# Kernel optimization log

Measured on AMD Instinct MI355X. Metric: run time of the kernel, lower is better.

## Reference

```python
import jax, jax.numpy as jnp
import numpy as np

NUM_HEADS = 16
KEY_DIM = 64
D_MODEL = 1024
SUPPORTS = 128


def _gaussian_orthogonal_random_matrix(m, d, seed=0):
    # GOR sampler with scaling=0: orthogonal blocks, rows rescaled by norms of iid Gaussian rows.
    rng = np.random.RandomState(seed)
    blocks = []
    n_full = m // d
    for _ in range(n_full):
        q, _ = np.linalg.qr(rng.randn(d, d))
        blocks.append(q.T)
    rem = m - n_full * d
    if rem > 0:
        q, _ = np.linalg.qr(rng.randn(d, d))
        blocks.append(q.T[:rem])
    W = np.concatenate(blocks, axis=0)  # [m, d], orthonormal rows per block
    multiplier = np.linalg.norm(rng.randn(m, d), axis=1)  # chi(d) row norms
    return (multiplier[:, None] * W).astype(np.float32)


def setup_inputs() -> dict:
    key0 = jax.random.key(0)
    ks = jax.random.split(key0, 12)
    B, S, D, H, K = 4, 4096, D_MODEL, NUM_HEADS, KEY_DIM
    glorot_in = lambda k, shape, fan_in, fan_out: jax.random.uniform(
        k, shape, jnp.float32, -1.0, 1.0) * np.sqrt(6.0 / (fan_in + fan_out))
    return {
        "query": jax.random.normal(ks[0], (B, S, D), jnp.float32),
        "value": jax.random.normal(ks[1], (B, S, D), jnp.float32),
        "key": jax.random.normal(ks[2], (B, S, D), jnp.float32),
        "Wq": glorot_in(ks[3], (D, H, K), D, H * K),
        "bq": jnp.zeros((H, K), jnp.float32),
        "Wk": glorot_in(ks[4], (D, H, K), D, H * K),
        "bk": jnp.zeros((H, K), jnp.float32),
        "Wv": glorot_in(ks[5], (D, H, K), D, H * K),
        "bv": jnp.zeros((H, K), jnp.float32),
        "Wo": glorot_in(ks[6], (H, K, D), H * K, D),
        "bo": jnp.zeros((D,), jnp.float32),
        "proj": jnp.asarray(_gaussian_orthogonal_random_matrix(SUPPORTS, K)),
    }


def kernel_feature_creator(data, projection, is_query):
    # FAVOR+ positive softmax-kernel features: phi(x) = exp(w.x' - |x'|^2/2 - stab)/sqrt(m)
    d = data.shape[-1]
    m = projection.shape[0]
    x = data * (d ** -0.25)  # so that q'.k' = q.k / sqrt(d)
    wx = jnp.einsum("bshk,mk->bshm", x, projection)
    diag = 0.5 * jnp.sum(x * x, axis=-1, keepdims=True)
    if is_query:
        stab = jax.lax.stop_gradient(jnp.max(wx, axis=-1, keepdims=True))
    else:
        stab = jax.lax.stop_gradient(jnp.max(wx))
    return jnp.exp(wx - diag - stab) * (m ** -0.5)


def reference(query, value, key, Wq, bq, Wk, bk, Wv, bv, Wo, bo, proj):
    # EinsumDense projections: [B,S,D] -> [B,S,H,K]
    q = jnp.einsum("bsd,dhk->bshk", query, Wq) + bq
    k = jnp.einsum("bsd,dhk->bshk", key, Wk) + bk
    v = jnp.einsum("bsd,dhk->bshk", value, Wv) + bv
    phi_q = kernel_feature_creator(q, proj, True)   # [B,T,H,M]
    phi_k = kernel_feature_creator(k, proj, False)  # [B,S,H,M]
    kv = jnp.einsum("bshm,bshd->bhmd", phi_k, v)
    qkv = jnp.einsum("bthm,bhmd->bthd", phi_q, kv)
    # normalisation: D = phi_q . (sum_s phi_k)
    k1 = jnp.sum(phi_k, axis=1)                     # [B,H,M]
    denom = jnp.einsum("bthm,bhm->bth", phi_q, k1)
    out = qkv * (1.0 / (denom + 1e-6))[..., None]
    return jnp.einsum("bthd,hdo->bto", out, Wo) + bo
```

## Files before the change

### kernel.cpp

```cpp
#include <hip/hip_runtime.h>
#include <hip/hip_bf16.h>


#define B_  4
#define S_  4096
#define H_  16

#define SCALE_X 0.3535533905932738f
#define CM      0.08838834764831845f

typedef __attribute__((ext_vector_type(8))) short bf16x8;
typedef __attribute__((ext_vector_type(4))) short s16x4;
typedef __attribute__((ext_vector_type(8))) unsigned short u16x8;
typedef __attribute__((ext_vector_type(8))) _Float16 f16x8;
typedef __attribute__((ext_vector_type(4))) _Float16 f16x4;
typedef __attribute__((ext_vector_type(4))) float f32x4;

#define OFF_A    ((size_t)0)
#define OFF_B    ((size_t)16777216)
#define OFF_X    ((size_t)33554432)
#define OFF_KV   ((size_t)37814272)
#define OFF_K1   ((size_t)38338560)
#define OFF_BM   ((size_t)38346752)
#define OFF_ST   ((size_t)38347264)
#define OFF_A16  ((size_t)38347776)

__device__ __forceinline__ unsigned short f2bf(float x) {
  union { __hip_bfloat16 b; unsigned short u; } c;
  c.b = __float2bfloat16(x);
  return c.u;
}

#define MFMAB(ACC, A, B)                                               \
  ACC = __builtin_amdgcn_mfma_f32_16x16x32_bf16(A, B, ACC, 0, 0, 0)

#define GLDS(GP, LP)                                                  \
  __builtin_amdgcn_global_load_lds(                                   \
      (const __attribute__((address_space(1))) unsigned int*)(GP),    \
      (__attribute__((address_space(3))) unsigned int*)(LP), 16, 0, 0)

__device__ __forceinline__ void load_pfrag(const float* __restrict__ proj, int m,
                                           int kb, bf16x8* ph) {
  const float* p = proj + m * 64 + kb;
  float4 a = *reinterpret_cast<const float4*>(p);
  float4 b = *reinterpret_cast<const float4*>(p + 4);
  float v[8] = {a.x, a.y, a.z, a.w, b.x, b.y, b.z, b.w};
  bf16x8 h;
#pragma unroll
  for (int j = 0; j < 8; ++j) h[j] = (short)f2bf(v[j]);
  *ph = h;
}

#define STAGE_XR(XV, WANT_DIAG)                                           \
  {                                                                       \
    f16x8 xv_ = (XV);                                                     \
    u16x8 hh_;                                                            \
    float sq_ = 0.f;                                                      \
    _Pragma("unroll") for (int j = 0; j < 8; ++j) {                       \
      float vf_ = (float)xv_[j] * SCALE_X;                                \
      sq_ += vf_ * vf_;                                                   \
      hh_[j] = f2bf(vf_);                                                 \
    }                                                                     \
    *reinterpret_cast<u16x8*>(&Xh[srow][xc]) = hh_;                       \
    if (WANT_DIAG) {                                                      \
      sq_ += __shfl_xor(sq_, 1);                                          \
      sq_ += __shfl_xor(sq_, 2);                                          \
      sq_ += __shfl_xor(sq_, 4);                                          \
      if ((tid & 7) == 0) diags[srow] = 0.5f * sq_;                       \
    }                                                                     \
  }

#define WX_COMPUTE(WX)                                                       \
  _Pragma("unroll") for (int st_ = 0; st_ < 2; ++st_)                        \
  _Pragma("unroll") for (int ks_ = 0; ks_ < 2; ++ks_) {                      \
    const int rr_ = st_ * 16 + l15;                                          \
    const int cc_ = ((ks_ * 4 + lg) ^ (l15 & 7)) << 3;                       \
    bf16x8 xh_ = *reinterpret_cast<const bf16x8*>(&Xh[rr_][cc_]);            \
    _Pragma("unroll") for (int mtl_ = 0; mtl_ < 2; ++mtl_)                   \
        MFMAB(WX[st_][mtl_], xh_, ph[mtl_][ks_]);                            \
  }

__global__ __launch_bounds__(256) void cvt_f16_kernel(
    const float* __restrict__ in, _Float16* __restrict__ out) {
  const size_t stride = (size_t)gridDim.x * 256 * 8;
  for (size_t i = ((size_t)blockIdx.x * 256 + threadIdx.x) * 8; i < 16777216UL;
       i += stride) {
    float4 a = *reinterpret_cast<const float4*>(in + i);
    float4 b = *reinterpret_cast<const float4*>(in + i + 4);
    f16x8 h;
    h[0] = (_Float16)a.x; h[1] = (_Float16)a.y;
    h[2] = (_Float16)a.z; h[3] = (_Float16)a.w;
    h[4] = (_Float16)b.x; h[5] = (_Float16)b.y;
    h[6] = (_Float16)b.z; h[7] = (_Float16)b.w;
    *reinterpret_cast<f16x8*>(out + i) = h;
  }
}

__global__ __launch_bounds__(256) void wt_f16_kernel(
    const float* __restrict__ W, _Float16* __restrict__ T) {
  __shared__ float t[32][33];
  const int tx = threadIdx.x & 31, ty = threadIdx.x >> 5;
  const int k0 = blockIdx.x * 32, n0 = blockIdx.y * 32;
#pragma unroll
  for (int i = 0; i < 4; ++i)
    t[ty + 8 * i][tx] = W[(size_t)(k0 + ty + 8 * i) * 1024 + n0 + tx];
  __syncthreads();
#pragma unroll
  for (int i = 0; i < 4; ++i)
    T[(size_t)(n0 + ty + 8 * i) * 1024 + k0 + tx] = (_Float16)t[tx][ty + 8 * i];
}

template <int F16OUT>
__global__ __launch_bounds__(512) void gemm_lds(
    const _Float16* __restrict__ A16, const _Float16* __restrict__ BT,
    const float* __restrict__ bias, void* __restrict__ Cout) {
  __shared__ _Float16 As[4][256][32];
  __shared__ _Float16 Bs[4][256][32];
  const int tid = threadIdx.x;
  const int bid = blockIdx.x;
  const int m0 = (bid & 63) << 8;
  const int n0 = (bid >> 6) << 8;
  const int wave = tid >> 6, lane = tid & 63;
  const int wm = (wave >> 2) << 7;
  const int wn = (wave & 3) << 6;
  const int l15 = lane & 15, lg = lane >> 4;

  const int rlo = tid >> 2;
  const int cg = ((tid & 3) ^ ((rlo >> 1) & 3)) << 3;
  const int wqbase = wave << 10;

  const _Float16* pa = A16 + (size_t)(m0 + rlo) * 1024 + cg;
  const _Float16* pb = BT + (size_t)(n0 + rlo) * 1024 + cg;

  f32x4 acc[8][4];
#pragma unroll
  for (int i = 0; i < 8; ++i)
#pragma unroll
    for (int j = 0; j < 4; ++j) acc[i][j] = f32x4{0.f, 0.f, 0.f, 0.f};

#define STAGE_T(nb, kt)                                                   \
  {                                                                       \
    char* la = (char*)&As[nb][0][0] + wqbase;                             \
    char* lb = (char*)&Bs[nb][0][0] + wqbase;                             \
    GLDS(pa + (kt) * 32, la);                                             \
    GLDS(pa + (kt) * 32 + 131072, la + 8192);                             \
    GLDS(pb + (kt) * 32, lb);                                             \
    GLDS(pb + (kt) * 32 + 131072, lb + 8192);                             \
  }

#define PIPE_BAR(N)                                                       \
  asm volatile("s_waitcnt vmcnt(" #N ")" ::: "memory");                   \
  __builtin_amdgcn_s_barrier();                                           \
  asm volatile("" ::: "memory");                                          \
  __builtin_amdgcn_sched_barrier(0);

#define COMPUTE(cur)                                                      \
  {                                                                       \
    f16x8 bf[4];                                                          \
    _Pragma("unroll") for (int fn = 0; fn < 4; ++fn) {                    \
      const int r = wn + fn * 16 + l15;                                   \
      bf[fn] = *reinterpret_cast<const f16x8*>(                           \
          &Bs[cur][r][(lg ^ ((r >> 1) & 3)) << 3]);                       \
    }                                                                     \
    _Pragma("unroll") for (int fm = 0; fm < 8; ++fm) {                    \
      const int r = wm + fm * 16 + l15;                                   \
      f16x8 av = *reinterpret_cast<const f16x8*>(                         \
          &As[cur][r][(lg ^ ((r >> 1) & 3)) << 3]);                       \
      _Pragma("unroll") for (int fn = 0; fn < 4; ++fn)                    \
        acc[fm][fn] = __builtin_amdgcn_mfma_f32_16x16x32_f16(             \
            av, bf[fn], acc[fm][fn], 0, 0, 0);                            \
    }                                                                     \
  }

  STAGE_T(0, 0);
  STAGE_T(1, 1);

  for (int kt = 0; kt < 30; ++kt) {
    STAGE_T((kt + 2) & 3, kt + 2);
    PIPE_BAR(8);
    COMPUTE(kt & 3);
  }
  PIPE_BAR(4);
  COMPUTE(2);
  PIPE_BAR(0);
  COMPUTE(3);

#pragma unroll
  for (int fm = 0; fm < 8; ++fm) {
    const int row = m0 + wm + fm * 16 + (lg << 2);
#pragma unroll
    for (int fn = 0; fn < 4; ++fn) {
      const int col = n0 + wn + fn * 16 + l15;
      const float bc = bias[col];
      f32x4 v = acc[fm][fn];
      if (F16OUT) {
        _Float16* C = (_Float16*)Cout;
#pragma unroll
        for (int j = 0; j < 4; ++j)
          C[(size_t)(row + j) * 1024 + col] = (_Float16)(v[j] + bc);
      } else {
        float* C = (float*)Cout;
#pragma unroll
        for (int j = 0; j < 4; ++j) C[(size_t)(row + j) * 1024 + col] = v[j] + bc;
      }
    }
  }
#undef STAGE_T
#undef PIPE_BAR
#undef COMPUTE
}

__global__ __launch_bounds__(256) void wxmax_mfma_kernel(
    const _Float16* __restrict__ kproj, const float* __restrict__ proj,
    float* __restrict__ blockmax) {
  __shared__ unsigned short Xh[32][64];
  __shared__ float diags[32];
  __shared__ float redw[4];
  const int tid = threadIdx.x, blk = blockIdx.x;
  const int lane = tid & 63, w = tid >> 6;
  const int l15 = lane & 15, lg = lane >> 4;
  (void)diags;

  bf16x8 ph[2][2];
#pragma unroll
  for (int mtl = 0; mtl < 2; ++mtl)
#pragma unroll
    for (int ks = 0; ks < 2; ++ks)
      load_pfrag(proj, (2 * w + mtl) * 16 + l15, ks * 32 + lg * 8, &ph[mtl][ks]);

  float gmax = -3.4e38f;
  const int srow = tid >> 3, q8 = (tid & 7) << 3;
  const int xc = ((q8 >> 3) ^ (srow & 7)) << 3;

  f16x8 xk = *reinterpret_cast<const f16x8*>(
      kproj + (size_t)(blk * 512 + srow) * 64 + q8);

  for (int batch = 0; batch < 16; ++batch) {
    STAGE_XR(xk, false);
    f16x8 xk2;
    if (batch < 15)
      xk2 = *reinterpret_cast<const f16x8*>(
          kproj + (size_t)(blk * 512 + (batch + 1) * 32 + srow) * 64 + q8);
    __syncthreads();
    f32x4 wx[2][2];
#pragma unroll
    for (int st = 0; st < 2; ++st)
#pragma unroll
      for (int mtl = 0; mtl < 2; ++mtl) wx[st][mtl] = f32x4{0, 0, 0, 0};
    WX_COMPUTE(wx);
#pragma unroll
    for (int st = 0; st < 2; ++st)
#pragma unroll
      for (int mtl = 0; mtl < 2; ++mtl)
#pragma unroll
        for (int r = 0; r < 4; ++r) gmax = fmaxf(gmax, wx[st][mtl][r]);
    __syncthreads();
    if (batch < 15) xk = xk2;
  }
#pragma unroll
  for (int off = 32; off; off >>= 1) gmax = fmaxf(gmax, __shfl_xor(gmax, off));
  if (lane == 0) redw[w] = gmax;
  __syncthreads();
  if (tid == 0)
    blockmax[blk] = fmaxf(fmaxf(redw[0], redw[1]), fmaxf(redw[2], redw[3]));
}

__global__ __launch_bounds__(256) void maxreduce_kernel(
    const float* __restrict__ blockmax, float* __restrict__ stab, int n) {
  __shared__ float sm[256];
  float v = -3.4e38f;
  for (int i = threadIdx.x; i < n; i += 256) v = fmaxf(v, blockmax[i]);
  sm[threadIdx.x] = v;
  __syncthreads();
  for (int s = 128; s; s >>= 1) {
    if (threadIdx.x < s)
      sm[threadIdx.x] = fmaxf(sm[threadIdx.x], sm[threadIdx.x + s]);
    __syncthreads();
  }
  if (threadIdx.x == 0) *stab = sm[0];
}

__global__ __launch_bounds__(256) void kv_mfma_kernel(
    const _Float16* __restrict__ kproj, const _Float16* __restrict__ vproj,
    const float* __restrict__ proj, const float* __restrict__ stabp,
    float* __restrict__ kvpartT, float* __restrict__ k1part) {
  __shared__ unsigned short Xh[32][64];
  __shared__ float Vs[32][66];
  __shared__ unsigned short phiTh[128][40];
  __shared__ float diags[32];
  const int tid = threadIdx.x, blk = blockIdx.x;
  const int c = blk & 15, bh = blk >> 4, b = bh >> 4, h = bh & 15;
  const int lane = tid & 63, w = tid >> 6;
  const int l15 = lane & 15, lg = lane >> 4;
  const float stab = *stabp;

  bf16x8 ph[2][2];
#pragma unroll
  for (int mtl = 0; mtl < 2; ++mtl)
#pragma unroll
    for (int ks = 0; ks < 2; ++ks)
      load_pfrag(proj, (2 * w + mtl) * 16 + l15, ks * 32 + lg * 8, &ph[mtl][ks]);

  f32x4 akv[2][4];
#pragma unroll
  for (int i = 0; i < 2; ++i)
#pragma unroll
    for (int j = 0; j < 4; ++j) akv[i][j] = f32x4{0, 0, 0, 0};
  float k1acc[2] = {0.f, 0.f};

  const int srow = tid >> 3, q8 = (tid & 7) << 3;
  const int xc = ((q8 >> 3) ^ (srow & 7)) << 3;

  size_t rb = (((size_t)(b * S_ + c * 256 + srow) * H_ + h)) << 6;
  f16x8 xk = *reinterpret_cast<const f16x8*>(kproj + rb + q8);
  f16x8 xv = *reinterpret_cast<const f16x8*>(vproj + rb + q8);

  for (int batch = 0; batch < 8; ++batch) {
    STAGE_XR(xk, true);
    {
#pragma unroll
      for (int j = 0; j < 8; ++j) Vs[srow][q8 + j] = (float)xv[j];
    }
    f16x8 xk2, xv2;
    if (batch < 7) {
      const size_t rb2 =
          (((size_t)(b * S_ + c * 256 + (batch + 1) * 32 + srow) * H_ + h)) << 6;
      xk2 = *reinterpret_cast<const f16x8*>(kproj + rb2 + q8);
      xv2 = *reinterpret_cast<const f16x8*>(vproj + rb2 + q8);
    }
    __syncthreads();

    f32x4 wx[2][2];
#pragma unroll
    for (int st = 0; st < 2; ++st)
#pragma unroll
      for (int mtl = 0; mtl < 2; ++mtl) wx[st][mtl] = f32x4{0, 0, 0, 0};
    WX_COMPUTE(wx);

#pragma unroll
    for (int st = 0; st < 2; ++st)
#pragma unroll
      for (int mtl = 0; mtl < 2; ++mtl) {
        const int m = (2 * w + mtl) * 16 + l15;
        s16x4 hv;
        float psum = 0.f;
#pragma unroll
        for (int r = 0; r < 4; ++r) {
          const int s = st * 16 + lg * 4 + r;
          float p = __expf(wx[st][mtl][r] - diags[s] - stab) * CM;
          psum += p;
          hv[r] = (short)f2bf(p);
        }
        k1acc[mtl] += psum;
        *reinterpret_cast<s16x4*>(&phiTh[m][st * 16 + lg * 4]) = hv;
      }
    __syncthreads();

    bf16x8 pah[2];
#pragma unroll
    for (int mtl = 0; mtl < 2; ++mtl)
      pah[mtl] = *reinterpret_cast<const bf16x8*>(
          &phiTh[(2 * w + mtl) * 16 + l15][lg * 8]);
#pragma unroll
    for (int dt = 0; dt < 4; ++dt) {
      bf16x8 bvh;
#pragma unroll
      for (int j = 0; j < 8; ++j)
        bvh[j] = (short)f2bf(Vs[lg * 8 + j][dt * 16 + l15]);
#pragma unroll
      for (int mtl = 0; mtl < 2; ++mtl) MFMAB(akv[mtl][dt], pah[mtl], bvh);
    }
    __syncthreads();
    if (batch < 7) {
      xk = xk2;
      xv = xv2;
    }
  }

#pragma unroll
  for (int mtl = 0; mtl < 2; ++mtl) {
#pragma unroll
    for (int dt = 0; dt < 4; ++dt) {
      const int d = dt * 16 + l15, m0 = (2 * w + mtl) * 16 + lg * 4;
      *reinterpret_cast<f32x4*>(&kvpartT[(size_t)blk * 8192 + d * 128 + m0]) =
          akv[mtl][dt];
    }
    float kk = k1acc[mtl];
    kk += __shfl_xor(kk, 16);
    kk += __shfl_xor(kk, 32);
    if (lane < 16) k1part[blk * 128 + (2 * w + mtl) * 16 + lane] = kk;
  }
}

__global__ __launch_bounds__(256) void kvreduce_kernel(
    const float* __restrict__ kvpartT, const float* __restrict__ k1part,
    unsigned short* __restrict__ kvT, float* __restrict__ k1) {
  const int bh = blockIdx.x;
  for (int i = threadIdx.x; i < 8192; i += 256) {
    float s = 0.f;
#pragma unroll
    for (int c = 0; c < 16; ++c) s += kvpartT[(size_t)(bh * 16 + c) * 8192 + i];
    kvT[(size_t)bh * 8192 + i] = f2bf(s);
  }
  if (threadIdx.x < 128) {
    float s = 0.f;
#pragma unroll
    for (int c = 0; c < 16; ++c) s += k1part[(bh * 16 + c) * 128 + threadIdx.x];
    k1[bh * 128 + threadIdx.x] = s;
  }
}

__global__ __launch_bounds__(256) void qkv_mfma_kernel(
    const _Float16* __restrict__ qproj, const unsigned short* __restrict__ kvT,
    const float* __restrict__ k1g, const float* __restrict__ proj,
    _Float16* __restrict__ outh) {
  __shared__ unsigned short Xh[32][64];
  __shared__ unsigned short Ph[32][128];
  __shared__ float k1s[128];
  __shared__ float diags[32];
  __shared__ float rmaxp[4][32];
  __shared__ float denp[4][32];
  const int tid = threadIdx.x, blk = blockIdx.x;
  const int ch = blk & 31, bh = blk >> 5, b = bh >> 4, h = bh & 15;
  const int lane = tid & 63, w = tid >> 6;
  const int l15 = lane & 15, lg = lane >> 4;

  bf16x8 ph[2][2];
#pragma unroll
  for (int mtl = 0; mtl < 2; ++mtl)
#pragma unroll
    for (int ks = 0; ks < 2; ++ks)
      load_pfrag(proj, (2 * w + mtl) * 16 + l15, ks * 32 + lg * 8, &ph[mtl][ks]);

  bf16x8 kah[4];
#pragma unroll
  for (int ks = 0; ks < 4; ++ks) {
    const size_t o = (size_t)bh * 8192 + (w * 16 + l15) * 128 + ks * 32 + lg * 8;
    kah[ks] = *reinterpret_cast<const bf16x8*>(kvT + o);
  }
  if (tid < 128) k1s[tid] = k1g[bh * 128 + tid];

  const int srow = tid >> 3, q8 = (tid & 7) << 3;
  const int xc = ((q8 >> 3) ^ (srow & 7)) << 3;

  f16x8 xpre[4];
#pragma unroll
  for (int batch = 0; batch < 4; ++batch) {
    const int s0 = ch * 128 + batch * 32;
    xpre[batch] = *reinterpret_cast<const f16x8*>(
        qproj + ((((size_t)(b * S_ + s0 + srow) * H_ + h)) << 6) + q8);
  }

#pragma unroll
  for (int batch = 0; batch < 4; ++batch) {
    const int s0 = ch * 128 + batch * 32;
    STAGE_XR(xpre[batch], true);
    __syncthreads();

    f32x4 wx[2][2];
#pragma unroll
    for (int st = 0; st < 2; ++st)
#pragma unroll
      for (int mtl = 0; mtl < 2; ++mtl) wx[st][mtl] = f32x4{0, 0, 0, 0};
    WX_COMPUTE(wx);

#pragma unroll
    for (int st = 0; st < 2; ++st)
#pragma unroll
      for (int r = 0; r < 4; ++r) {
        float v = fmaxf(wx[st][0][r], wx[st][1][r]);
        v = fmaxf(v, __shfl_xor(v, 1));
        v = fmaxf(v, __shfl_xor(v, 2));
        v = fmaxf(v, __shfl_xor(v, 4));
        v = fmaxf(v, __shfl_xor(v, 8));
        if (l15 == 0) rmaxp[w][st * 16 + lg * 4 + r] = v;
      }
    __syncthreads();

#pragma unroll
    for (int st = 0; st < 2; ++st) {
      float off[4];
#pragma unroll
      for (int r = 0; r < 4; ++r) {
        const int s = st * 16 + lg * 4 + r;
        float rmx = fmaxf(fmaxf(rmaxp[0][s], rmaxp[1][s]),
                          fmaxf(rmaxp[2][s], rmaxp[3][s]));
        off[r] = rmx + diags[s];
      }
      float den[4] = {0.f, 0.f, 0.f, 0.f};
#pragma unroll
      for (int mtl = 0; mtl < 2; ++mtl) {
        const int m = (2 * w + mtl) * 16 + l15;
        const float k1v = k1s[m];
#pragma unroll
        for (int r = 0; r < 4; ++r) {
          const int s = st * 16 + lg * 4 + r;
          float p = __expf(wx[st][mtl][r] - off[r]) * CM;
          den[r] += p * k1v;
          Ph[s][((((m >> 3) ^ (s & 7)) << 3) | (m & 7))] = f2bf(p);
        }
      }
#pragma unroll
      for (int r = 0; r < 4; ++r) {
        float v = den[r];
        v += __shfl_xor(v, 1);
        v += __shfl_xor(v, 2);
        v += __shfl_xor(v, 4);
        v += __shfl_xor(v, 8);
        if (l15 == 0) denp[w][st * 16 + lg * 4 + r] = v;
      }
    }
    __syncthreads();

#pragma unroll
    for (int st = 0; st < 2; ++st) {
      f32x4 od = {0.f, 0.f, 0.f, 0.f};
#pragma unroll
      for (int ks = 0; ks < 4; ++ks) {
        const int cc = ((ks * 4 + lg) ^ (l15 & 7)) << 3;
        bf16x8 bph = *reinterpret_cast<const bf16x8*>(&Ph[st * 16 + l15][cc]);
        MFMAB(od, kah[ks], bph);
      }
      const int s = st * 16 + l15;
      const float dens =
          1.f / (denp[0][s] + denp[1][s] + denp[2][s] + denp[3][s] + 1e-6f);
      f16x4 o;
#pragma unroll
      for (int j = 0; j < 4; ++j) o[j] = (_Float16)(od[j] * dens);
      *reinterpret_cast<f16x4*>(
          &outh[(size_t)(b * S_ + s0 + s) * 1024 + h * 64 + w * 16 + lg * 4]) = o;
    }
    __syncthreads();
  }
}

extern "C" void kernel_launch(void* const* d_in, const int* in_sizes, int n_in,
                              void* d_out, int out_size, void* d_ws,
                              size_t ws_size, hipStream_t stream) {
  const float* query = (const float*)d_in[0];
  const float* value = (const float*)d_in[1];
  const float* key   = (const float*)d_in[2];
  const float* Wq = (const float*)d_in[3];
  const float* bq = (const float*)d_in[4];
  const float* Wk = (const float*)d_in[5];
  const float* bk = (const float*)d_in[6];
  const float* Wv = (const float*)d_in[7];
  const float* bv = (const float*)d_in[8];
  const float* Wo = (const float*)d_in[9];
  const float* bo = (const float*)d_in[10];
  const float* proj = (const float*)d_in[11];
  float* out = (float*)d_out;
  float* ws = (float*)d_ws;

  _Float16* KP16 = (_Float16*)(ws + OFF_A);
  _Float16* VP16 = (_Float16*)(ws + OFF_B);
  _Float16* WT = (_Float16*)(ws + OFF_X);
  float* K1P = ws + OFF_X;
  unsigned short* KVT = (unsigned short*)(ws + OFF_KV);
  float* K1 = ws + OFF_K1;
  float* BMX = ws + OFF_BM;
  float* ST = ws + OFF_ST;
  _Float16* X16 = (_Float16*)(ws + OFF_A16);
  float* KVPT = ws + OFF_A16;

  dim3 gw(32, 32);

  cvt_f16_kernel<<<2048, 256, 0, stream>>>(key, X16);
  wt_f16_kernel<<<gw, 256, 0, stream>>>(Wk, WT);
  gemm_lds<1><<<256, 512, 0, stream>>>(X16, WT, bk, KP16);
  wxmax_mfma_kernel<<<512, 256, 0, stream>>>(KP16, proj, BMX);
  maxreduce_kernel<<<1, 256, 0, stream>>>(BMX, ST, 512);
  cvt_f16_kernel<<<2048, 256, 0, stream>>>(value, X16);
  wt_f16_kernel<<<gw, 256, 0, stream>>>(Wv, WT);
  gemm_lds<1><<<256, 512, 0, stream>>>(X16, WT, bv, VP16);
  kv_mfma_kernel<<<1024, 256, 0, stream>>>(KP16, VP16, proj, ST, KVPT, K1P);
  kvreduce_kernel<<<64, 256, 0, stream>>>(KVPT, K1P, KVT, K1);
  cvt_f16_kernel<<<2048, 256, 0, stream>>>(query, X16);
  wt_f16_kernel<<<gw, 256, 0, stream>>>(Wq, WT);
  gemm_lds<1><<<256, 512, 0, stream>>>(X16, WT, bq, KP16);
  qkv_mfma_kernel<<<2048, 256, 0, stream>>>(KP16, KVT, K1, proj, X16);
  wt_f16_kernel<<<gw, 256, 0, stream>>>(Wo, WT);
  gemm_lds<0><<<256, 512, 0, stream>>>(X16, WT, bo, out);
}
```

Before: 328.4 us.

## Restructure query-feature kernel so each wave owns full rows without block barriers

The qkv kernel is reorganised so each wave handles 16 query rows across all 128 features, instead of four waves splitting the feature dimension of 32-row batches. This removes the cross-wave row-max and denominator exchanges and the per-batch __syncthreads. The projection and kv matrices are staged once in LDS, with a swizzle, and read from there rather than held in registers. Per-wave register use grows (8 accumulator tiles), and the per-wave LDS writes and reads of P have no explicit wave barrier, so they depend on lockstep execution within the wave.

```diff
diff --git a/kernel.cpp b/kernel.cpp
--- a/kernel.cpp
+++ b/kernel.cpp
@@ -410,127 +410,138 @@
   }
 }
 
-__global__ __launch_bounds__(256) void qkv_mfma_kernel(
+__global__ __launch_bounds__(256) void qkv_wave_kernel(
     const _Float16* __restrict__ qproj, const unsigned short* __restrict__ kvT,
     const float* __restrict__ k1g, const float* __restrict__ proj,
     _Float16* __restrict__ outh) {
-  __shared__ unsigned short Xh[32][64];
-  __shared__ unsigned short Ph[32][128];
+  __shared__ unsigned short Pl[128][64];
+  __shared__ unsigned short Kl[64][128];
+  __shared__ unsigned short Phw[4][16][128];
   __shared__ float k1s[128];
-  __shared__ float diags[32];
-  __shared__ float rmaxp[4][32];
-  __shared__ float denp[4][32];
+  __shared__ float dgw[4][16];
+  __shared__ float dnw[4][16];
   const int tid = threadIdx.x, blk = blockIdx.x;
   const int ch = blk & 31, bh = blk >> 5, b = bh >> 4, h = bh & 15;
   const int lane = tid & 63, w = tid >> 6;
   const int l15 = lane & 15, lg = lane >> 4;
 
-  bf16x8 ph[2][2];
-#pragma unroll
-  for (int mtl = 0; mtl < 2; ++mtl)
-#pragma unroll
-    for (int ks = 0; ks < 2; ++ks)
-      load_pfrag(proj, (2 * w + mtl) * 16 + l15, ks * 32 + lg * 8, &ph[mtl][ks]);
-
-  bf16x8 kah[4];
-#pragma unroll
-  for (int ks = 0; ks < 4; ++ks) {
-    const size_t o = (size_t)bh * 8192 + (w * 16 + l15) * 128 + ks * 32 + lg * 8;
-    kah[ks] = *reinterpret_cast<const bf16x8*>(kvT + o);
-  }
-  if (tid < 128) k1s[tid] = k1g[bh * 128 + tid];
-
-  const int srow = tid >> 3, q8 = (tid & 7) << 3;
-  const int xc = ((q8 >> 3) ^ (srow & 7)) << 3;
-
-  f16x8 xpre[4];
-#pragma unroll
-  for (int batch = 0; batch < 4; ++batch) {
-    const int s0 = ch * 128 + batch * 32;
-    xpre[batch] = *reinterpret_cast<const f16x8*>(
-        qproj + ((((size_t)(b * S_ + s0 + srow) * H_ + h)) << 6) + q8);
-  }
-
-#pragma unroll
-  for (int batch = 0; batch < 4; ++batch) {
-    const int s0 = ch * 128 + batch * 32;
-    STAGE_XR(xpre[batch], true);
-    __syncthreads();
-
-    f32x4 wx[2][2];
-#pragma unroll
-    for (int st = 0; st < 2; ++st)
-#pragma unroll
-      for (int mtl = 0; mtl < 2; ++mtl) wx[st][mtl] = f32x4{0, 0, 0, 0};
-    WX_COMPUTE(wx);
-
-#pragma unroll
-    for (int st = 0; st < 2; ++st)
-#pragma unroll
-      for (int r = 0; r < 4; ++r) {
-        float v = fmaxf(wx[st][0][r], wx[st][1][r]);
-        v = fmaxf(v, __shfl_xor(v, 1));
-        v = fmaxf(v, __shfl_xor(v, 2));
-        v = fmaxf(v, __shfl_xor(v, 4));
-        v = fmaxf(v, __shfl_xor(v, 8));
-        if (l15 == 0) rmaxp[w][st * 16 + lg * 4 + r] = v;
+  {
+    const int r = tid >> 1;
+    const int cb = (tid & 1) << 2;
+#pragma unroll
+    for (int j = 0; j < 4; ++j) {
+      const int ck = cb + j;
+      float4 a = *reinterpret_cast<const float4*>(proj + r * 64 + ck * 8);
+      float4 bq = *reinterpret_cast<const float4*>(proj + r * 64 + ck * 8 + 4);
+      float v[8] = {a.x, a.y, a.z, a.w, bq.x, bq.y, bq.z, bq.w};
+      u16x8 hh;
+#pragma unroll
+      for (int q = 0; q < 8; ++q) hh[q] = f2bf(v[q]);
+      *reinterpret_cast<u16x8*>(&Pl[r][(ck ^ (r & 7)) << 3]) = hh;
+    }
+    const int d = tid >> 2;
+    const int kb = (tid & 3) << 2;
+#pragma unroll
+    for (int j = 0; j < 4; ++j) {
+      const int ck = kb + j;
+      u16x8 kk = *reinterpret_cast<const u16x8*>(
+          kvT + (size_t)bh * 8192 + d * 128 + ck * 8);
+      *reinterpret_cast<u16x8*>(&Kl[d][(ck ^ (d & 7)) << 3]) = kk;
+    }
+    if (tid < 128) k1s[tid] = k1g[bh * 128 + tid];
+  }
+  __syncthreads();
+
+  float k1v[8];
+#pragma unroll
+  for (int mt = 0; mt < 8; ++mt) k1v[mt] = k1s[mt * 16 + l15];
+
+#pragma unroll
+  for (int it = 0; it < 2; ++it) {
+    const int t0 = ch * 128 + w * 32 + it * 16;
+    const size_t xrow = (((size_t)(b * S_ + t0 + l15) * H_ + h)) << 6;
+    f16x8 x0 = *reinterpret_cast<const f16x8*>(qproj + xrow + lg * 8);
+    f16x8 x1 = *reinterpret_cast<const f16x8*>(qproj + xrow + 32 + lg * 8);
+    bf16x8 xb0, xb1;
+    float sq = 0.f;
+#pragma unroll
+    for (int j = 0; j < 8; ++j) {
+      float v0 = (float)x0[j] * SCALE_X;
+      float v1 = (float)x1[j] * SCALE_X;
+      sq += v0 * v0 + v1 * v1;
+      xb0[j] = (short)f2bf(v0);
+      xb1[j] = (short)f2bf(v1);
+    }
+    sq += __shfl_xor(sq, 16);
+    sq += __shfl_xor(sq, 32);
+    if (lg == 0) dgw[w][l15] = 0.5f * sq;
+
+    f32x4 wxa[8];
+#pragma unroll
+    for (int mt = 0; mt < 8; ++mt) {
+      wxa[mt] = f32x4{0.f, 0.f, 0.f, 0.f};
+      bf16x8 p0 = *reinterpret_cast<const bf16x8*>(
+          &Pl[mt * 16 + l15][((lg) ^ (l15 & 7)) << 3]);
+      bf16x8 p1 = *reinterpret_cast<const bf16x8*>(
+          &Pl[mt * 16 + l15][((4 + lg) ^ (l15 & 7)) << 3]);
+      MFMAB(wxa[mt], xb0, p0);
+      MFMAB(wxa[mt], xb1, p1);
+    }
+
+    float rmx[4];
+#pragma unroll
+    for (int r = 0; r < 4; ++r) {
+      float v = wxa[0][r];
+#pragma unroll
+      for (int mt = 1; mt < 8; ++mt) v = fmaxf(v, wxa[mt][r]);
+      v = fmaxf(v, __shfl_xor(v, 1));
+      v = fmaxf(v, __shfl_xor(v, 2));
+      v = fmaxf(v, __shfl_xor(v, 4));
+      v = fmaxf(v, __shfl_xor(v, 8));
+      rmx[r] = v;
+    }
+    float den[4] = {0.f, 0.f, 0.f, 0.f};
+#pragma unroll
+    for (int r = 0; r < 4; ++r) {
+      const int trow = lg * 4 + r;
+      const float off = rmx[r] + dgw[w][trow];
+#pragma unroll
+      for (int mt = 0; mt < 8; ++mt) {
+        const int m = mt * 16 + l15;
+        float p = __expf(wxa[mt][r] - off) * CM;
+        den[r] += p * k1v[mt];
+        Phw[w][trow][((((m >> 3)) ^ (trow & 7)) << 3) | (m & 7)] = f2bf(p);
       }
-    __syncthreads();
-
-#pragma unroll
-    for (int st = 0; st < 2; ++st) {
-      float off[4];
-#pragma unroll
-      for (int r = 0; r < 4; ++r) {
-        const int s = st * 16 + lg * 4 + r;
-        float rmx = fmaxf(fmaxf(rmaxp[0][s], rmaxp[1][s]),
-                          fmaxf(rmaxp[2][s], rmaxp[3][s]));
-        off[r] = rmx + diags[s];
+    }
+#pragma unroll
+    for (int r = 0; r < 4; ++r) {
+      float v = den[r];
+      v += __shfl_xor(v, 1);
+      v += __shfl_xor(v, 2);
+      v += __shfl_xor(v, 4);
+      v += __shfl_xor(v, 8);
+      if (l15 == 0) dnw[w][lg * 4 + r] = v;
+    }
+
+    const float dens = 1.f / (dnw[w][l15] + 1e-6f);
+#pragma unroll
+    for (int dt = 0; dt < 4; ++dt) {
+      f32x4 od = {0.f, 0.f, 0.f, 0.f};
+#pragma unroll
+      for (int ks = 0; ks < 4; ++ks) {
+        bf16x8 ka = *reinterpret_cast<const bf16x8*>(
+            &Kl[dt * 16 + l15][((ks * 4 + lg) ^ (l15 & 7)) << 3]);
+        bf16x8 bp = *reinterpret_cast<const bf16x8*>(
+            &Phw[w][l15][((ks * 4 + lg) ^ (l15 & 7)) << 3]);
+        MFMAB(od, ka, bp);
       }
-      float den[4] = {0.f, 0.f, 0.f, 0.f};
-#pragma unroll
-      for (int mtl = 0; mtl < 2; ++mtl) {
-        const int m = (2 * w + mtl) * 16 + l15;
-        const float k1v = k1s[m];
-#pragma unroll
-        for (int r = 0; r < 4; ++r) {
-          const int s = st * 16 + lg * 4 + r;
-          float p = __expf(wx[st][mtl][r] - off[r]) * CM;
-          den[r] += p * k1v;
-          Ph[s][((((m >> 3) ^ (s & 7)) << 3) | (m & 7))] = f2bf(p);
-        }
-      }
-#pragma unroll
-      for (int r = 0; r < 4; ++r) {
-        float v = den[r];
-        v += __shfl_xor(v, 1);
-        v += __shfl_xor(v, 2);
-        v += __shfl_xor(v, 4);
-        v += __shfl_xor(v, 8);
-        if (l15 == 0) denp[w][st * 16 + lg * 4 + r] = v;
-      }
-    }
-    __syncthreads();
-
-#pragma unroll
-    for (int st = 0; st < 2; ++st) {
-      f32x4 od = {0.f, 0.f, 0.f, 0.f};
-#pragma unroll
-      for (int ks = 0; ks < 4; ++ks) {
-        const int cc = ((ks * 4 + lg) ^ (l15 & 7)) << 3;
-        bf16x8 bph = *reinterpret_cast<const bf16x8*>(&Ph[st * 16 + l15][cc]);
-        MFMAB(od, kah[ks], bph);
-      }
-      const int s = st * 16 + l15;
-      const float dens =
-          1.f / (denp[0][s] + denp[1][s] + denp[2][s] + denp[3][s] + 1e-6f);
       f16x4 o;
 #pragma unroll
       for (int j = 0; j < 4; ++j) o[j] = (_Float16)(od[j] * dens);
       *reinterpret_cast<f16x4*>(
-          &outh[(size_t)(b * S_ + s0 + s) * 1024 + h * 64 + w * 16 + lg * 4]) = o;
-    }
-    __syncthreads();
+          &outh[(size_t)(b * S_ + t0 + l15) * 1024 + h * 64 + dt * 16 +
+                lg * 4]) = o;
+    }
   }
 }
 
@@ -578,7 +589,7 @@
   cvt_f16_kernel<<<2048, 256, 0, stream>>>(query, X16);
   wt_f16_kernel<<<gw, 256, 0, stream>>>(Wq, WT);
   gemm_lds<1><<<256, 512, 0, stream>>>(X16, WT, bq, KP16);
-  qkv_mfma_kernel<<<2048, 256, 0, stream>>>(KP16, KVT, K1, proj, X16);
+  qkv_wave_kernel<<<2048, 256, 0, stream>>>(KP16, KVT, K1, proj, X16);
   wt_f16_kernel<<<gw, 256, 0, stream>>>(Wo, WT);
   gemm_lds<0><<<256, 512, 0, stream>>>(X16, WT, bo, out);
 }
```

After: 301.7 us, median of 2. 8.1% less time.
